# Kernel optimization log

Hardware: AMD Instinct MI355X
Metric: run time of the kernel (lower is better)

The kernel has to match this reference:

```python
import jax, jax.numpy as jnp
import numpy as np

B, T, H, A = 64, 512, 1024, 300


def setup_inputs() -> dict:
    key = jax.random.key(0)
    ks = jax.random.split(key, 12)
    s = 0.02  # weight init scale
    return {
        "hidden": jax.random.normal(ks[0], (B, T, H), jnp.float32),
        "aspect": jax.random.normal(ks[1], (B, 1, A), jnp.float32),
        # torch Linear stores weight as [out_features, in_features]
        "W_h": jax.random.normal(ks[2], (H, H), jnp.float32) * s,
        "b_h": jax.random.normal(ks[3], (H,), jnp.float32) * s,
        "W_v": jax.random.normal(ks[4], (A, A), jnp.float32) * s,
        "b_v": jax.random.normal(ks[5], (A,), jnp.float32) * s,
        "w_w": jax.random.normal(ks[6], (1, H + A), jnp.float32) * s,
        "w_b": jax.random.normal(ks[7], (1,), jnp.float32) * s,
        "W_p": jax.random.normal(ks[8], (H, H), jnp.float32) * s,
        "b_p": jax.random.normal(ks[9], (H,), jnp.float32) * s,
        "W_x": jax.random.normal(ks[10], (H, H), jnp.float32) * s,
        "b_x": jax.random.normal(ks[11], (H,), jnp.float32) * s,
    }


def reference(hidden, aspect, W_h, b_h, W_v, b_v, w_w, w_b, W_p, b_p, W_x, b_x):
    # transformed aspect: [B, 1, A], repeated along seq dim -> [B, T, A]
    tv = aspect @ W_v.T + b_v
    rep_v = jnp.broadcast_to(tv, (hidden.shape[0], hidden.shape[1], tv.shape[-1]))
    # M = tanh(concat(W_h(hidden), repeated_v)) : [B, T, H+A]
    M = jnp.tanh(jnp.concatenate([hidden @ W_h.T + b_h, rep_v], axis=-1))
    # additive attention scores -> softmax over T
    scores = jnp.einsum("bts,os->bto", M, w_w)[..., 0] + w_b[0]  # [B, T]
    alpha = jax.nn.softmax(scores, axis=-1)
    # weighted sum r = alpha^T @ hidden : [B, 1, H]
    r = jnp.einsum("bt,bth->bh", alpha, hidden)[:, None, :]
    # NOTE: faithful to original torch broadcasting quirk:
    # [B,1,H] + [B,H] broadcasts to [B,B,H]
    output = jnp.tanh((r @ W_p.T + b_p) + (hidden[:, -1, :] @ W_x.T + b_x))
    return output
```

## Files before the change

kernel.cpp:

```cpp
#include <hip/hip_runtime.h>
#include <hip/hip_bf16.h>
#include <stdint.h>

#define B_DIM 64
#define T_DIM 512
#define H_DIM 1024
#define K_DIM 1024
#define M_DIM (B_DIM * T_DIM)

typedef __bf16 bf16x8 __attribute__((ext_vector_type(8)));
typedef float f32x4 __attribute__((ext_vector_type(4)));

__device__ __forceinline__ float tanh_fast(float x) {
  float e = __expf(2.0f * x);
  return 1.0f - 2.0f / (e + 1.0f);
}

__device__ __forceinline__ float bf2f(unsigned short u) {
  return __uint_as_float(((unsigned int)u) << 16);
}

__device__ __forceinline__ void async_cp16(const void* gp, void* lp) {
  __builtin_amdgcn_global_load_lds(
      reinterpret_cast<const __attribute__((address_space(1))) uint32_t*>(
          reinterpret_cast<uintptr_t>(gp)),
      reinterpret_cast<__attribute__((address_space(3))) uint32_t*>(
          reinterpret_cast<uintptr_t>(lp)),
      16, 0, 0);
}

__global__ void cvt_hidden_kernel(const float* __restrict__ src, __bf16* __restrict__ dst) {
  int i = blockIdx.x * 256 + threadIdx.x;
  float4 v = reinterpret_cast<const float4*>(src)[i];
  union { __bf16 b[4]; uint2 u; } o;
  o.b[0] = (__bf16)v.x; o.b[1] = (__bf16)v.y; o.b[2] = (__bf16)v.z; o.b[3] = (__bf16)v.w;
  reinterpret_cast<uint2*>(dst)[i] = o.u;
}

__global__ void cvtW_zero_kernel(const float* __restrict__ Wh, __bf16* __restrict__ whBf,
                                 float* __restrict__ scores, float* __restrict__ r) {
  int bid = blockIdx.x, tid = threadIdx.x;
  if (bid < 1024) {
    int i = bid * 256 + tid;
    float4 v = reinterpret_cast<const float4*>(Wh)[i];
    union { __bf16 b[4]; uint2 u; } o;
    o.b[0] = (__bf16)v.x; o.b[1] = (__bf16)v.y; o.b[2] = (__bf16)v.z; o.b[3] = (__bf16)v.w;
    reinterpret_cast<uint2*>(whBf)[i] = o.u;
  } else if (bid < 1056) {
    int i = (bid - 1024) * 256 + tid;
    reinterpret_cast<float4*>(scores)[i] = make_float4(0.f, 0.f, 0.f, 0.f);
  } else {
    int i = (bid - 1056) * 256 + tid;
    reinterpret_cast<float4*>(r)[i] = make_float4(0.f, 0.f, 0.f, 0.f);
  }
}

#define GM_BK 64
__global__ __launch_bounds__(256, 2) void gemm_scores_kernel(
    const __bf16* __restrict__ A, const __bf16* __restrict__ Bm,
    const float* __restrict__ bh, const float* __restrict__ ww,
    float* __restrict__ scores) {
  __shared__ __attribute__((aligned(16))) __bf16 lA[256 * GM_BK];
  __shared__ __attribute__((aligned(16))) __bf16 lB[128 * GM_BK];

  const int tid = threadIdx.x;
  const int bid = blockIdx.x;
  const int m0 = (bid & 127) * 256;
  const int n0 = (bid >> 7) * 128;

  const int wv = tid >> 6;
  const int lane = tid & 63;
  const int wm = wv & 1, wn = wv >> 1;
  const int r16 = lane & 15, quad = lane >> 4;

  f32x4 acc[8][4] = {};

  const __bf16* gA[8]; __bf16* lAd[8];
#pragma unroll
  for (int j = 0; j < 8; ++j) {
    int c = j * 256 + tid;
    int row = c >> 3;
    int p = c & 7;
    int kc = p ^ ((row >> 1) & 7);
    gA[j] = A + (size_t)(m0 + row) * K_DIM + kc * 8;
    lAd[j] = &lA[c * 8];
  }
  const __bf16* gB[4]; __bf16* lBd[4];
#pragma unroll
  for (int j = 0; j < 4; ++j) {
    int c = j * 256 + tid;
    int row = c >> 3;
    int p = c & 7;
    int kc = p ^ ((row >> 1) & 7);
    gB[j] = Bm + (size_t)(n0 + row) * K_DIM + kc * 8;
    lBd[j] = &lB[c * 8];
  }

  const int sw = r16 >> 1;
  const __bf16* pa[2]; const __bf16* pb[2];
#pragma unroll
  for (int kk = 0; kk < 2; ++kk) {
    pa[kk] = &lA[(wm * 128 + r16) * GM_BK + ((kk * 4 + quad) ^ sw) * 8];
    pb[kk] = &lB[(wn * 64 + r16) * GM_BK + ((kk * 4 + quad) ^ sw) * 8];
  }

#pragma unroll
  for (int k0 = 0; k0 < K_DIM; k0 += GM_BK) {
#pragma unroll
    for (int j = 0; j < 8; ++j) async_cp16(gA[j] + k0, lAd[j]);
#pragma unroll
    for (int j = 0; j < 4; ++j) async_cp16(gB[j] + k0, lBd[j]);
    __syncthreads();
#pragma unroll
    for (int kk = 0; kk < 2; ++kk) {
      bf16x8 bfr[4];
#pragma unroll
      for (int ni = 0; ni < 4; ++ni)
        bfr[ni] = *reinterpret_cast<const bf16x8*>(pb[kk] + ni * 16 * GM_BK);
      bf16x8 af[8];
#pragma unroll
      for (int mi = 0; mi < 8; ++mi)
        af[mi] = *reinterpret_cast<const bf16x8*>(pa[kk] + mi * 16 * GM_BK);
#pragma unroll
      for (int mi = 0; mi < 8; ++mi)
#pragma unroll
        for (int ni = 0; ni < 4; ++ni)
          acc[mi][ni] = __builtin_amdgcn_mfma_f32_16x16x32_bf16(af[mi], bfr[ni], acc[mi][ni], 0, 0, 0);
    }
    __syncthreads();
  }

  float bhv[4], wwv[4];
#pragma unroll
  for (int ni = 0; ni < 4; ++ni) {
    int n = n0 + wn * 64 + ni * 16 + r16;
    bhv[ni] = bh[n];
    wwv[ni] = ww[n];
  }
#pragma unroll
  for (int mi = 0; mi < 8; ++mi) {
#pragma unroll
    for (int rg = 0; rg < 4; ++rg) {
      float s = 0.f;
#pragma unroll
      for (int ni = 0; ni < 4; ++ni)
        s += tanh_fast(acc[mi][ni][rg] + bhv[ni]) * wwv[ni];
      s += __shfl_xor(s, 1, 16);
      s += __shfl_xor(s, 2, 16);
      s += __shfl_xor(s, 4, 16);
      s += __shfl_xor(s, 8, 16);
      if (r16 == 0) {
        int m = m0 + wm * 128 + mi * 16 + quad * 4 + rg;
        atomicAdd(&scores[m], s);
      }
    }
  }
}

__global__ void wsum_kernel(const float* __restrict__ scores,
                            const __bf16* __restrict__ hiddenBf,
                            float* __restrict__ r) {
  __shared__ float al[64];
  __shared__ float red[8];
  const int bid = blockIdx.x, tid = threadIdx.x;
  const int b = bid >> 3, tc = bid & 7;
  const int wv = tid >> 6, lane = tid & 63;
  float v0 = scores[b * T_DIM + tid];
  float v1 = scores[b * T_DIM + 256 + tid];
  float mx = fmaxf(v0, v1);
#pragma unroll
  for (int off = 1; off < 64; off <<= 1) mx = fmaxf(mx, __shfl_xor(mx, off, 64));
  if (lane == 0) red[wv] = mx;
  __syncthreads();
  mx = fmaxf(fmaxf(red[0], red[1]), fmaxf(red[2], red[3]));
  float e0 = __expf(v0 - mx), e1 = __expf(v1 - mx);
  float s = e0 + e1;
#pragma unroll
  for (int off = 1; off < 64; off <<= 1) s += __shfl_xor(s, off, 64);
  if (lane == 0) red[4 + wv] = s;
  __syncthreads();
  float inv = 1.0f / (red[4] + red[5] + red[6] + red[7]);
  if (tid < 64) al[tid] = __expf(scores[b * T_DIM + tc * 64 + tid] - mx) * inv;
  __syncthreads();
  const __bf16* hp = hiddenBf + (size_t)b * T_DIM * H_DIM + (size_t)tc * 64 * H_DIM + tid * 4;
  float4 acc = make_float4(0.f, 0.f, 0.f, 0.f);
#pragma unroll 8
  for (int t = 0; t < 64; ++t) {
    float a = al[t];
    ushort4 u = *reinterpret_cast<const ushort4*>(hp + (size_t)t * H_DIM);
    acc.x += a * bf2f(u.x);
    acc.y += a * bf2f(u.y);
    acc.z += a * bf2f(u.z);
    acc.w += a * bf2f(u.w);
  }
  float* rp = r + b * H_DIM + tid * 4;
  atomicAdd(rp + 0, acc.x);
  atomicAdd(rp + 1, acc.y);
  atomicAdd(rp + 2, acc.z);
  atomicAdd(rp + 3, acc.w);
}

__global__ void rowvec_matT_kernel(const float* __restrict__ src, size_t src_stride,
                                   const float* __restrict__ W, const float* __restrict__ bias,
                                   float* __restrict__ dst) {
  __shared__ float sv[H_DIM];
  const int i = blockIdx.y, h0 = blockIdx.x * 64, tid = threadIdx.x;
  reinterpret_cast<float4*>(sv)[tid] =
      reinterpret_cast<const float4*>(src + (size_t)i * src_stride)[tid];
  __syncthreads();
  const int hl = tid >> 2;
  const int kq = tid & 3;
  const float* wr = W + (size_t)(h0 + hl) * H_DIM + kq * 256;
  const float* svp = sv + kq * 256;
  float acc = 0.f;
#pragma unroll 4
  for (int k = 0; k < 256; k += 4) {
    float4 w4 = *reinterpret_cast<const float4*>(wr + k);
    float4 s4 = *reinterpret_cast<const float4*>(svp + k);
    acc += w4.x * s4.x + w4.y * s4.y + w4.z * s4.z + w4.w * s4.w;
  }
  acc += __shfl_xor(acc, 1, 4);
  acc += __shfl_xor(acc, 2, 4);
  if (kq == 0) dst[(size_t)i * H_DIM + h0 + hl] = acc + bias[h0 + hl];
}

__global__ void final_kernel(const float* __restrict__ rp, const float* __restrict__ xq,
                             float* __restrict__ out) {
  int idx = blockIdx.x * 256 + threadIdx.x;
  int e = idx * 4;
  int i = e >> 16;
  int j = (e >> 10) & 63;
  int h = e & 1023;
  float4 a = *reinterpret_cast<const float4*>(&rp[i * H_DIM + h]);
  float4 b = *reinterpret_cast<const float4*>(&xq[j * H_DIM + h]);
  float4 o;
  o.x = tanh_fast(a.x + b.x);
  o.y = tanh_fast(a.y + b.y);
  o.z = tanh_fast(a.z + b.z);
  o.w = tanh_fast(a.w + b.w);
  *reinterpret_cast<float4*>(&out[e]) = o;
}

extern "C" void kernel_launch(void* const* d_in, const int* in_sizes, int n_in,
                              void* d_out, int out_size, void* d_ws, size_t ws_size,
                              hipStream_t stream) {
  const float* hidden = (const float*)d_in[0];
  const float* W_h = (const float*)d_in[2];
  const float* b_h = (const float*)d_in[3];
  const float* w_w = (const float*)d_in[6];
  const float* W_p = (const float*)d_in[8];
  const float* b_p = (const float*)d_in[9];
  const float* W_x = (const float*)d_in[10];
  const float* b_x = (const float*)d_in[11];
  float* out = (float*)d_out;

  char* ws = (char*)d_ws;
  __bf16* hidBf = (__bf16*)ws;
  __bf16* whBf = (__bf16*)(ws + 67108864);
  float* scores = (float*)(ws + 69206016);
  float* r = (float*)(ws + 69468160);
  float* rp = (float*)(ws + 69730304);
  float* xq = (float*)(ws + 69992448);

  cvt_hidden_kernel<<<M_DIM * H_DIM / 1024, 256, 0, stream>>>(hidden, hidBf);
  cvtW_zero_kernel<<<1072, 256, 0, stream>>>(W_h, whBf, scores, r);

  gemm_scores_kernel<<<1024, 256, 0, stream>>>(hidBf, whBf, b_h, w_w, scores);

  wsum_kernel<<<512, 256, 0, stream>>>(scores, hidBf, r);

  rowvec_matT_kernel<<<dim3(H_DIM / 64, B_DIM), 256, 0, stream>>>(r, (size_t)H_DIM, W_p, b_p, rp);
  rowvec_matT_kernel<<<dim3(H_DIM / 64, B_DIM), 256, 0, stream>>>(
      hidden + (size_t)(T_DIM - 1) * H_DIM, (size_t)T_DIM * H_DIM, W_x, b_x, xq);

  final_kernel<<<(B_DIM * B_DIM * H_DIM / 4) / 256, 256, 0, stream>>>(rp, xq, out);
}
```

Before: 383.6 us.

## Switch hidden and W_h intermediate storage and GEMM to scaled FP8 MFMA

Hidden and W_h are now stored as FP8 E4M3 with fixed power-of-two prescales (16 and 32) instead of bf16. The score GEMM moves from bf16 16x16x32 MFMA to the scaled 32x32x64 f8f6f4 MFMA, whose block scales undo the prescales, and the LDS tiles are laid out again for that operand format. The weighted-sum kernel reads FP8 hidden and rescales by 1/16. This halves the bytes moved by conversion, GEMM loads and the weighted sum, and doubles MFMA throughput. The cost is much lower precision for the attention scores and the weighted sum, which could break tolerance.

```diff
diff --git a/kernel.cpp b/kernel.cpp
--- a/kernel.cpp
+++ b/kernel.cpp
@@ -8,16 +8,14 @@
 #define K_DIM 1024
 #define M_DIM (B_DIM * T_DIM)
 
-typedef __bf16 bf16x8 __attribute__((ext_vector_type(8)));
-typedef float f32x4 __attribute__((ext_vector_type(4)));
+typedef int i32x4 __attribute__((ext_vector_type(4)));
+typedef int i32x8 __attribute__((ext_vector_type(8)));
+typedef float f32x2 __attribute__((ext_vector_type(2)));
+typedef float f32x16 __attribute__((ext_vector_type(16)));
 
 __device__ __forceinline__ float tanh_fast(float x) {
   float e = __expf(2.0f * x);
   return 1.0f - 2.0f / (e + 1.0f);
-}
-
-__device__ __forceinline__ float bf2f(unsigned short u) {
-  return __uint_as_float(((unsigned int)u) << 16);
 }
 
 __device__ __forceinline__ void async_cp16(const void* gp, void* lp) {
@@ -29,23 +27,23 @@
       16, 0, 0);
 }
 
-__global__ void cvt_hidden_kernel(const float* __restrict__ src, __bf16* __restrict__ dst) {
+__global__ void cvt_hidden_kernel(const float* __restrict__ src, int* __restrict__ dst) {
   int i = blockIdx.x * 256 + threadIdx.x;
   float4 v = reinterpret_cast<const float4*>(src)[i];
-  union { __bf16 b[4]; uint2 u; } o;
-  o.b[0] = (__bf16)v.x; o.b[1] = (__bf16)v.y; o.b[2] = (__bf16)v.z; o.b[3] = (__bf16)v.w;
-  reinterpret_cast<uint2*>(dst)[i] = o.u;
-}
-
-__global__ void cvtW_zero_kernel(const float* __restrict__ Wh, __bf16* __restrict__ whBf,
+  int d = __builtin_amdgcn_cvt_pk_fp8_f32(v.x * 16.f, v.y * 16.f, 0, false);
+  d = __builtin_amdgcn_cvt_pk_fp8_f32(v.z * 16.f, v.w * 16.f, d, true);
+  dst[i] = d;
+}
+
+__global__ void cvtW_zero_kernel(const float* __restrict__ Wh, int* __restrict__ whF8,
                                  float* __restrict__ scores, float* __restrict__ r) {
   int bid = blockIdx.x, tid = threadIdx.x;
   if (bid < 1024) {
     int i = bid * 256 + tid;
     float4 v = reinterpret_cast<const float4*>(Wh)[i];
-    union { __bf16 b[4]; uint2 u; } o;
-    o.b[0] = (__bf16)v.x; o.b[1] = (__bf16)v.y; o.b[2] = (__bf16)v.z; o.b[3] = (__bf16)v.w;
-    reinterpret_cast<uint2*>(whBf)[i] = o.u;
+    int d = __builtin_amdgcn_cvt_pk_fp8_f32(v.x * 32.f, v.y * 32.f, 0, false);
+    d = __builtin_amdgcn_cvt_pk_fp8_f32(v.z * 32.f, v.w * 32.f, d, true);
+    whF8[i] = d;
   } else if (bid < 1056) {
     int i = (bid - 1024) * 256 + tid;
     reinterpret_cast<float4*>(scores)[i] = make_float4(0.f, 0.f, 0.f, 0.f);
@@ -57,11 +55,11 @@
 
 #define GM_BK 64
 __global__ __launch_bounds__(256, 2) void gemm_scores_kernel(
-    const __bf16* __restrict__ A, const __bf16* __restrict__ Bm,
+    const uint8_t* __restrict__ Af8, const uint8_t* __restrict__ Bf8,
     const float* __restrict__ bh, const float* __restrict__ ww,
     float* __restrict__ scores) {
-  __shared__ __attribute__((aligned(16))) __bf16 lA[256 * GM_BK];
-  __shared__ __attribute__((aligned(16))) __bf16 lB[128 * GM_BK];
+  __shared__ __attribute__((aligned(16))) uint8_t lA[256 * GM_BK];
+  __shared__ __attribute__((aligned(16))) uint8_t lB[128 * GM_BK];
 
   const int tid = threadIdx.x;
   const int bid = blockIdx.x;
@@ -71,86 +69,87 @@
   const int wv = tid >> 6;
   const int lane = tid & 63;
   const int wm = wv & 1, wn = wv >> 1;
-  const int r16 = lane & 15, quad = lane >> 4;
-
-  f32x4 acc[8][4] = {};
-
-  const __bf16* gA[8]; __bf16* lAd[8];
-#pragma unroll
-  for (int j = 0; j < 8; ++j) {
+  const int r32 = lane & 31, khalf = lane >> 5;
+
+  f32x16 acc[4][2] = {};
+
+  const uint8_t* gA[4]; uint8_t* lAd[4];
+#pragma unroll
+  for (int j = 0; j < 4; ++j) {
+    gA[j] = Af8 + (size_t)(m0 + tid) * K_DIM + j * 16;
+    lAd[j] = &lA[(j * 256 + tid) * 16];
+  }
+  const uint8_t* gB[2]; uint8_t* lBd[2];
+#pragma unroll
+  for (int j = 0; j < 2; ++j) {
     int c = j * 256 + tid;
-    int row = c >> 3;
-    int p = c & 7;
-    int kc = p ^ ((row >> 1) & 7);
-    gA[j] = A + (size_t)(m0 + row) * K_DIM + kc * 8;
-    lAd[j] = &lA[c * 8];
-  }
-  const __bf16* gB[4]; __bf16* lBd[4];
-#pragma unroll
-  for (int j = 0; j < 4; ++j) {
-    int c = j * 256 + tid;
-    int row = c >> 3;
-    int p = c & 7;
-    int kc = p ^ ((row >> 1) & 7);
-    gB[j] = Bm + (size_t)(n0 + row) * K_DIM + kc * 8;
-    lBd[j] = &lB[c * 8];
-  }
-
-  const int sw = r16 >> 1;
-  const __bf16* pa[2]; const __bf16* pb[2];
-#pragma unroll
-  for (int kk = 0; kk < 2; ++kk) {
-    pa[kk] = &lA[(wm * 128 + r16) * GM_BK + ((kk * 4 + quad) ^ sw) * 8];
-    pb[kk] = &lB[(wn * 64 + r16) * GM_BK + ((kk * 4 + quad) ^ sw) * 8];
-  }
+    int row = c & 127, kc = c >> 7;
+    gB[j] = Bf8 + (size_t)(n0 + row) * K_DIM + kc * 16;
+    lBd[j] = &lB[c * 16];
+  }
+
+  const uint8_t* paf[4];
+#pragma unroll
+  for (int mi = 0; mi < 4; ++mi)
+    paf[mi] = &lA[((khalf * 2) * 256 + wm * 128 + mi * 32 + r32) * 16];
+  const uint8_t* pbf[2];
+#pragma unroll
+  for (int ni = 0; ni < 2; ++ni)
+    pbf[ni] = &lB[((khalf * 2) * 128 + wn * 64 + ni * 32 + r32) * 16];
 
 #pragma unroll
   for (int k0 = 0; k0 < K_DIM; k0 += GM_BK) {
 #pragma unroll
-    for (int j = 0; j < 8; ++j) async_cp16(gA[j] + k0, lAd[j]);
-#pragma unroll
-    for (int j = 0; j < 4; ++j) async_cp16(gB[j] + k0, lBd[j]);
+    for (int j = 0; j < 4; ++j) async_cp16(gA[j] + k0, lAd[j]);
+#pragma unroll
+    for (int j = 0; j < 2; ++j) async_cp16(gB[j] + k0, lBd[j]);
     __syncthreads();
-#pragma unroll
-    for (int kk = 0; kk < 2; ++kk) {
-      bf16x8 bfr[4];
-#pragma unroll
-      for (int ni = 0; ni < 4; ++ni)
-        bfr[ni] = *reinterpret_cast<const bf16x8*>(pb[kk] + ni * 16 * GM_BK);
-      bf16x8 af[8];
-#pragma unroll
-      for (int mi = 0; mi < 8; ++mi)
-        af[mi] = *reinterpret_cast<const bf16x8*>(pa[kk] + mi * 16 * GM_BK);
-#pragma unroll
-      for (int mi = 0; mi < 8; ++mi)
-#pragma unroll
-        for (int ni = 0; ni < 4; ++ni)
-          acc[mi][ni] = __builtin_amdgcn_mfma_f32_16x16x32_bf16(af[mi], bfr[ni], acc[mi][ni], 0, 0, 0);
+
+    i32x8 bfr[2];
+#pragma unroll
+    for (int ni = 0; ni < 2; ++ni) {
+      i32x4 lo = *reinterpret_cast<const i32x4*>(pbf[ni]);
+      i32x4 hi = *reinterpret_cast<const i32x4*>(pbf[ni] + 128 * 16);
+      bfr[ni] = __builtin_shufflevector(lo, hi, 0, 1, 2, 3, 4, 5, 6, 7);
     }
+    i32x8 af[4];
+#pragma unroll
+    for (int mi = 0; mi < 4; ++mi) {
+      i32x4 lo = *reinterpret_cast<const i32x4*>(paf[mi]);
+      i32x4 hi = *reinterpret_cast<const i32x4*>(paf[mi] + 256 * 16);
+      af[mi] = __builtin_shufflevector(lo, hi, 0, 1, 2, 3, 4, 5, 6, 7);
+    }
+#pragma unroll
+    for (int mi = 0; mi < 4; ++mi)
+#pragma unroll
+      for (int ni = 0; ni < 2; ++ni)
+        acc[mi][ni] = __builtin_amdgcn_mfma_scale_f32_32x32x64_f8f6f4(
+            af[mi], bfr[ni], acc[mi][ni], 0, 0,
+            0, 0x7B7B7B7B,
+            0, 0x7A7A7A7A);
     __syncthreads();
   }
 
-  float bhv[4], wwv[4];
-#pragma unroll
-  for (int ni = 0; ni < 4; ++ni) {
-    int n = n0 + wn * 64 + ni * 16 + r16;
+  float bhv[2], wwv[2];
+#pragma unroll
+  for (int ni = 0; ni < 2; ++ni) {
+    int n = n0 + wn * 64 + ni * 32 + r32;
     bhv[ni] = bh[n];
     wwv[ni] = ww[n];
   }
 #pragma unroll
-  for (int mi = 0; mi < 8; ++mi) {
-#pragma unroll
-    for (int rg = 0; rg < 4; ++rg) {
-      float s = 0.f;
-#pragma unroll
-      for (int ni = 0; ni < 4; ++ni)
-        s += tanh_fast(acc[mi][ni][rg] + bhv[ni]) * wwv[ni];
-      s += __shfl_xor(s, 1, 16);
-      s += __shfl_xor(s, 2, 16);
-      s += __shfl_xor(s, 4, 16);
-      s += __shfl_xor(s, 8, 16);
-      if (r16 == 0) {
-        int m = m0 + wm * 128 + mi * 16 + quad * 4 + rg;
+  for (int mi = 0; mi < 4; ++mi) {
+#pragma unroll
+    for (int rg = 0; rg < 16; ++rg) {
+      float s = tanh_fast(acc[mi][0][rg] + bhv[0]) * wwv[0] +
+                tanh_fast(acc[mi][1][rg] + bhv[1]) * wwv[1];
+      s += __shfl_xor(s, 1, 32);
+      s += __shfl_xor(s, 2, 32);
+      s += __shfl_xor(s, 4, 32);
+      s += __shfl_xor(s, 8, 32);
+      s += __shfl_xor(s, 16, 32);
+      if (r32 == 0) {
+        int m = m0 + wm * 128 + mi * 32 + (rg & 3) + 8 * (rg >> 2) + 4 * khalf;
         atomicAdd(&scores[m], s);
       }
     }
@@ -158,7 +157,7 @@
 }
 
 __global__ void wsum_kernel(const float* __restrict__ scores,
-                            const __bf16* __restrict__ hiddenBf,
+                            const uint8_t* __restrict__ hidF8,
                             float* __restrict__ r) {
   __shared__ float al[64];
   __shared__ float red[8];
@@ -182,22 +181,25 @@
   float inv = 1.0f / (red[4] + red[5] + red[6] + red[7]);
   if (tid < 64) al[tid] = __expf(scores[b * T_DIM + tc * 64 + tid] - mx) * inv;
   __syncthreads();
-  const __bf16* hp = hiddenBf + (size_t)b * T_DIM * H_DIM + (size_t)tc * 64 * H_DIM + tid * 4;
+  const int* hp = reinterpret_cast<const int*>(hidF8) +
+                  ((size_t)b * T_DIM * H_DIM + (size_t)tc * 64 * H_DIM) / 4 + tid;
   float4 acc = make_float4(0.f, 0.f, 0.f, 0.f);
 #pragma unroll 8
   for (int t = 0; t < 64; ++t) {
     float a = al[t];
-    ushort4 u = *reinterpret_cast<const ushort4*>(hp + (size_t)t * H_DIM);
-    acc.x += a * bf2f(u.x);
-    acc.y += a * bf2f(u.y);
-    acc.z += a * bf2f(u.z);
-    acc.w += a * bf2f(u.w);
+    int u = hp[t * (H_DIM / 4)];
+    f32x2 lo = __builtin_amdgcn_cvt_pk_f32_fp8(u, false);
+    f32x2 hi = __builtin_amdgcn_cvt_pk_f32_fp8(u, true);
+    acc.x += a * lo[0];
+    acc.y += a * lo[1];
+    acc.z += a * hi[0];
+    acc.w += a * hi[1];
   }
   float* rp = r + b * H_DIM + tid * 4;
-  atomicAdd(rp + 0, acc.x);
-  atomicAdd(rp + 1, acc.y);
-  atomicAdd(rp + 2, acc.z);
-  atomicAdd(rp + 3, acc.w);
+  atomicAdd(rp + 0, acc.x * 0.0625f);
+  atomicAdd(rp + 1, acc.y * 0.0625f);
+  atomicAdd(rp + 2, acc.z * 0.0625f);
+  atomicAdd(rp + 3, acc.w * 0.0625f);
 }
 
 __global__ void rowvec_matT_kernel(const float* __restrict__ src, size_t src_stride,
@@ -255,19 +257,19 @@
   float* out = (float*)d_out;
 
   char* ws = (char*)d_ws;
-  __bf16* hidBf = (__bf16*)ws;
-  __bf16* whBf = (__bf16*)(ws + 67108864);
-  float* scores = (float*)(ws + 69206016);
-  float* r = (float*)(ws + 69468160);
-  float* rp = (float*)(ws + 69730304);
-  float* xq = (float*)(ws + 69992448);
-
-  cvt_hidden_kernel<<<M_DIM * H_DIM / 1024, 256, 0, stream>>>(hidden, hidBf);
-  cvtW_zero_kernel<<<1072, 256, 0, stream>>>(W_h, whBf, scores, r);
-
-  gemm_scores_kernel<<<1024, 256, 0, stream>>>(hidBf, whBf, b_h, w_w, scores);
-
-  wsum_kernel<<<512, 256, 0, stream>>>(scores, hidBf, r);
+  uint8_t* hidF8 = (uint8_t*)ws;
+  uint8_t* whF8 = (uint8_t*)(ws + 33554432);
+  float* scores = (float*)(ws + 34603008);
+  float* r = (float*)(ws + 34734080);
+  float* rp = (float*)(ws + 34996224);
+  float* xq = (float*)(ws + 35258368);
+
+  cvt_hidden_kernel<<<32768, 256, 0, stream>>>(hidden, (int*)hidF8);
+  cvtW_zero_kernel<<<1120, 256, 0, stream>>>(W_h, (int*)whF8, scores, r);
+
+  gemm_scores_kernel<<<1024, 256, 0, stream>>>(hidF8, whF8, b_h, w_w, scores);
+
+  wsum_kernel<<<512, 256, 0, stream>>>(scores, hidF8, r);
 
   rowvec_matT_kernel<<<dim3(H_DIM / 64, B_DIM), 256, 0, stream>>>(r, (size_t)H_DIM, W_p, b_p, rp);
   rowvec_matT_kernel<<<dim3(H_DIM / 64, B_DIM), 256, 0, stream>>>(
```

Result: slower. 627.6 us (+63.6%).
